# Performance work log

Measured on AMD Instinct MI355X. Metric: run time of the kernel, lower is better.

The kernel has to match this reference:

```python
import jax, jax.numpy as jnp
import numpy as np

B, M = 512, 2048            # batch of src-tgt pairs, sampled walk positions per pair
NUM_KEYS = 1_000_000        # unique (node, time) keys in nodetime2emb map
NUM_NODES = 100_000
LP = 4                      # num_layers + 1 (saw encoding width)
ENC = 32                    # enc_dim
FEAT = 64                   # node feature dim (MergeLayer dim2)
D3, D4 = 64, 1              # MergeLayer hidden / output dims


def setup_inputs() -> dict:
    key = jax.random.key(0)
    ks = jax.random.split(key, 12)
    s = 0.05
    return {
        "pos_table": jax.random.uniform(ks[0], (NUM_KEYS, LP), dtype=jnp.float32),
        "node_feat": jax.random.normal(ks[1], (NUM_NODES, FEAT), dtype=jnp.float32),
        "W1": jax.random.normal(ks[2], (LP, ENC), dtype=jnp.float32) * s,
        "b1": jnp.zeros((ENC,), dtype=jnp.float32),
        "W2": jax.random.normal(ks[3], (ENC, ENC), dtype=jnp.float32) * s,
        "b2": jnp.zeros((ENC,), dtype=jnp.float32),
        "Wm1": jax.random.normal(ks[4], (ENC + FEAT, D3), dtype=jnp.float32) * s,
        "bm1": jnp.zeros((D3,), dtype=jnp.float32),
        "Wm2": jax.random.normal(ks[5], (D3, D4), dtype=jnp.float32) * s,
        "bm2": jnp.zeros((D4,), dtype=jnp.float32),
        "key_idx": jax.random.randint(ks[6], (B, M), 0, NUM_KEYS, dtype=jnp.int32),
        "node_idx": jax.random.randint(ks[7], (B, M), 0, NUM_NODES, dtype=jnp.int32),
    }


def reference(pos_table, node_feat, W1, b1, W2, b2, Wm1, bm1, Wm2, bm2, key_idx, node_idx):
    # PositionEncoder.forward: gather saw encodings by (node, time) key,
    # then trainable_embedding = Linear(LP->ENC) -> ReLU -> Linear(ENC->ENC)
    enc = pos_table[key_idx]                       # [B, M, LP] irregular gather
    pe = jax.nn.relu(enc @ W1 + b1) @ W2 + b2      # [B, M, ENC]
    # gather raw node features for the same walk positions
    feat = node_feat[node_idx]                     # [B, M, FEAT] irregular gather
    # MergeLayer (non_linear=True): concat -> fc1 -> ReLU -> fc2
    x = jnp.concatenate([pe, feat], axis=-1)       # [B, M, ENC+FEAT]
    z = jax.nn.relu(x @ Wm1 + bm1) @ Wm2 + bm2     # [B, M, 1]
    return z
```

## Files before the change

kernel.cpp:

```cpp
#include <hip/hip_runtime.h>


typedef _Float16 half8 __attribute__((ext_vector_type(8)));
typedef float floatx4 __attribute__((ext_vector_type(4)));

#define HSTR 40
#define WSTR 104
#define GRID_MAIN 768

__global__ void feat_to_f16(const float* __restrict__ nf,
                            _Float16* __restrict__ o, int n8) {
    int t = blockIdx.x * 256 + threadIdx.x;
    if (t >= n8) return;
    const float4* p = (const float4*)nf + (size_t)t * 2;
    const float4 a = p[0], b = p[1];
    half8 h;
    h[0] = (_Float16)a.x; h[1] = (_Float16)a.y;
    h[2] = (_Float16)a.z; h[3] = (_Float16)a.w;
    h[4] = (_Float16)b.x; h[5] = (_Float16)b.y;
    h[6] = (_Float16)b.z; h[7] = (_Float16)b.w;
    *((half8*)o + t) = h;
}

__device__ __forceinline__ void load_feat(const _Float16* __restrict__ feat16,
                                          const float* __restrict__ node_feat,
                                          int use_f16, const int* ndr, int q,
                                          half8 fA[4][2]) {
    if (use_f16) {
        #pragma unroll
        for (int rt = 0; rt < 4; ++rt) {
            const _Float16* fb = feat16 + (size_t)ndr[rt] * 64 + q * 8;
            fA[rt][0] = *(const half8*)(fb);
            fA[rt][1] = *(const half8*)(fb + 32);
        }
    } else {
        #pragma unroll
        for (int rt = 0; rt < 4; ++rt) {
            const float* fb = node_feat + (size_t)ndr[rt] * 64 + q * 8;
            #pragma unroll
            for (int kt = 0; kt < 2; ++kt) {
                const float4 lo = *(const float4*)(fb + kt * 32);
                const float4 hi = *(const float4*)(fb + kt * 32 + 4);
                half8 h;
                h[0] = (_Float16)lo.x; h[1] = (_Float16)lo.y;
                h[2] = (_Float16)lo.z; h[3] = (_Float16)lo.w;
                h[4] = (_Float16)hi.x; h[5] = (_Float16)hi.y;
                h[6] = (_Float16)hi.z; h[7] = (_Float16)hi.w;
                fA[rt][kt] = h;
            }
        }
    }
}

__global__ __launch_bounds__(256, 3) void neurtw_r14(
    const float* __restrict__ pos_table,
    const float* __restrict__ node_feat,
    const float* __restrict__ W1,
    const float* __restrict__ b1,
    const float* __restrict__ W2,
    const float* __restrict__ b2,
    const float* __restrict__ Wm1,
    const float* __restrict__ bm1,
    const float* __restrict__ Wm2,
    const float* __restrict__ bm2,
    const int*   __restrict__ key_idx,
    const int*   __restrict__ node_idx,
    const _Float16* __restrict__ feat16,
    int use_f16,
    float*       __restrict__ out,
    int rows)
{
    __shared__ _Float16 hpe[256 * HSTR];
    __shared__ _Float16 wm1t[64 * WSTR];

    const int tid  = threadIdx.x;
    const int lane = tid & 63;
    const int r0   = (tid >> 6) * 64;
    const int ln   = lane & 15;
    const int q    = lane >> 4;

    #pragma unroll
    for (int i = 0; i < 3; ++i) {
        const int task = i * 256 + tid;
        const int n = task & 63, k8 = task >> 6;
        half8 w;
        #pragma unroll
        for (int kk = 0; kk < 8; ++kk)
            w[kk] = (_Float16)Wm1[(k8 * 8 + kk) * 64 + n];
        *(half8*)(&wm1t[n * WSTR + k8 * 8]) = w;
    }

    half8 b_w2[2];
    #pragma unroll
    for (int ct = 0; ct < 2; ++ct)
        #pragma unroll
        for (int j = 0; j < 8; ++j)
            b_w2[ct][j] = (_Float16)W2[(q * 8 + j) * 32 + ct * 16 + ln];
    float b2v[2];
    b2v[0] = b2[ln]; b2v[1] = b2[16 + ln];
    float bm1v[4], wm2v[4];
    #pragma unroll
    for (int ct = 0; ct < 4; ++ct) {
        bm1v[ct] = bm1[ct * 16 + ln];
        wm2v[ct] = Wm2[ct * 16 + ln];
    }
    const float bm2s = bm2[0];

    __syncthreads();

    int base = blockIdx.x * 256;
    int ndr[4];
    #pragma unroll
    for (int rt = 0; rt < 4; ++rt)
        ndr[rt] = node_idx[base + r0 + rt * 16 + ln];
    int kkc = key_idx[base + tid];
    float4 enc = *(const float4*)(pos_table + (size_t)kkc * 4);

    while (base < rows) {
        const int nbase = base + GRID_MAIN * 256;
        const bool more = nbase < rows;

        half8 fA[4][2];
        load_feat(feat16, node_feat, use_f16, ndr, q, fA);

        int ndr_n[4];
        int kk_n;
        if (more) {
            #pragma unroll
            for (int rt = 0; rt < 4; ++rt)
                ndr_n[rt] = node_idx[nbase + r0 + rt * 16 + ln];
            kk_n = key_idx[nbase + tid];
        } else {
            #pragma unroll
            for (int rt = 0; rt < 4; ++rt)
                ndr_n[rt] = 0;
            kk_n = 0;
        }

        #pragma unroll
        for (int g = 0; g < 4; ++g) {
            half8 hv;
            #pragma unroll
            for (int j8 = 0; j8 < 8; ++j8) {
                const int j = g * 8 + j8;
                float a = fmaf(enc.w, W1[96 + j],
                          fmaf(enc.z, W1[64 + j],
                          fmaf(enc.y, W1[32 + j],
                          fmaf(enc.x, W1[j], b1[j]))));
                hv[j8] = (_Float16)fmaxf(a, 0.0f);
            }
            *(half8*)(&hpe[tid * HSTR + g * 8]) = hv;
        }
        half8 a_h[4];
        #pragma unroll
        for (int rt = 0; rt < 4; ++rt)
            a_h[rt] = *(const half8*)(&hpe[(r0 + rt * 16 + ln) * HSTR + q * 8]);

        floatx4 pc[4][2];
        #pragma unroll
        for (int rt = 0; rt < 4; ++rt)
            #pragma unroll
            for (int ct = 0; ct < 2; ++ct) {
                floatx4 c = {0.f, 0.f, 0.f, 0.f};
                pc[rt][ct] = __builtin_amdgcn_mfma_f32_16x16x32_f16(
                    a_h[rt], b_w2[ct], c, 0, 0, 0);
            }

        #pragma unroll
        for (int rt = 0; rt < 4; ++rt)
            #pragma unroll
            for (int ct = 0; ct < 2; ++ct)
                #pragma unroll
                for (int r = 0; r < 4; ++r)
                    hpe[(r0 + rt * 16 + q * 4 + r) * HSTR + ct * 16 + ln] =
                        (_Float16)(pc[rt][ct][r] + b2v[ct]);

        float4 enc_n = enc;
        if (more)
            enc_n = *(const float4*)(pos_table + (size_t)kk_n * 4);

        floatx4 acc[4][4];
        #pragma unroll
        for (int ct = 0; ct < 4; ++ct) {
            const float bb = bm1v[ct];
            #pragma unroll
            for (int rt = 0; rt < 4; ++rt)
                acc[rt][ct] = (floatx4){bb, bb, bb, bb};
        }

        {
            half8 a_pe[4];
            #pragma unroll
            for (int rt = 0; rt < 4; ++rt)
                a_pe[rt] = *(const half8*)(&hpe[(r0 + rt * 16 + ln) * HSTR + q * 8]);
            half8 b0[4];
            #pragma unroll
            for (int ct = 0; ct < 4; ++ct)
                b0[ct] = *(const half8*)(&wm1t[(ct * 16 + ln) * WSTR + q * 8]);
            #pragma unroll
            for (int rt = 0; rt < 4; ++rt)
                #pragma unroll
                for (int ct = 0; ct < 4; ++ct)
                    acc[rt][ct] = __builtin_amdgcn_mfma_f32_16x16x32_f16(
                        a_pe[rt], b0[ct], acc[rt][ct], 0, 0, 0);
        }

        #pragma unroll
        for (int kt = 0; kt < 2; ++kt) {
            half8 bk[4];
            #pragma unroll
            for (int ct = 0; ct < 4; ++ct)
                bk[ct] = *(const half8*)(&wm1t[(ct * 16 + ln) * WSTR + 32 + kt * 32 + q * 8]);
            #pragma unroll
            for (int rt = 0; rt < 4; ++rt)
                #pragma unroll
                for (int ct = 0; ct < 4; ++ct)
                    acc[rt][ct] = __builtin_amdgcn_mfma_f32_16x16x32_f16(
                        fA[rt][kt], bk[ct], acc[rt][ct], 0, 0, 0);
        }

        #pragma unroll
        for (int rt = 0; rt < 4; ++rt) {
            #pragma unroll
            for (int r = 0; r < 4; ++r) {
                float p = 0.0f;
                #pragma unroll
                for (int ct = 0; ct < 4; ++ct)
                    p = fmaf(fmaxf(acc[rt][ct][r], 0.0f), wm2v[ct], p);
                p += __shfl_xor(p, 1);
                p += __shfl_xor(p, 2);
                p += __shfl_xor(p, 4);
                p += __shfl_xor(p, 8);
                if (ln == 0)
                    out[base + r0 + rt * 16 + q * 4 + r] = p + bm2s;
            }
        }

        base = nbase;
        #pragma unroll
        for (int rt = 0; rt < 4; ++rt)
            ndr[rt] = ndr_n[rt];
        kkc = kk_n;
        enc = enc_n;
    }
}

extern "C" void kernel_launch(void* const* d_in, const int* in_sizes, int n_in,
                              void* d_out, int out_size, void* d_ws, size_t ws_size,
                              hipStream_t stream) {
    const float* pos_table = (const float*)d_in[0];
    const float* node_feat = (const float*)d_in[1];
    const float* W1        = (const float*)d_in[2];
    const float* b1        = (const float*)d_in[3];
    const float* W2        = (const float*)d_in[4];
    const float* b2        = (const float*)d_in[5];
    const float* Wm1       = (const float*)d_in[6];
    const float* bm1       = (const float*)d_in[7];
    const float* Wm2       = (const float*)d_in[8];
    const float* bm2       = (const float*)d_in[9];
    const int*   key_idx   = (const int*)d_in[10];
    const int*   node_idx  = (const int*)d_in[11];
    float* out = (float*)d_out;

    const int rows  = in_sizes[10];
    const int nfeat = in_sizes[1];

    _Float16* feat16 = (_Float16*)d_ws;
    const size_t need = (size_t)nfeat * sizeof(_Float16);
    const int use_f16 = (ws_size >= need) ? 1 : 0;

    if (use_f16) {
        const int n8 = nfeat / 8;
        feat_to_f16<<<(n8 + 255) / 256, 256, 0, stream>>>(node_feat, feat16, n8);
    }

    neurtw_r14<<<GRID_MAIN, 256, 0, stream>>>(
        pos_table, node_feat, W1, b1, W2, b2, Wm1, bm1, Wm2, bm2,
        key_idx, node_idx, feat16, use_f16, out, rows);
}
```

Baseline: 156.8 us.

## Split MLP into two half-tiles to cut registers and raise occupancy

Splits the per-wave work of 4 row tiles into two passes of 2 row tiles, so the feature fragments and fc1 accumulators need only half the registers. The gather for the second half is issued in the middle of the first half's MFMAs. Launch bounds go from 3 to 4 waves per SIMD and the persistent grid from 768 to 1024 blocks, aiming to hide the random gather latency with more waves in flight. The cost is extra shared-memory B-fragment reloads and a more serialized instruction stream within each wave.

```diff
diff --git a/kernel.cpp b/kernel.cpp
--- a/kernel.cpp
+++ b/kernel.cpp
@@ -6,7 +6,7 @@
 
 #define HSTR 40
 #define WSTR 104
-#define GRID_MAIN 768
+#define GRID_MAIN 1024
 
 __global__ void feat_to_f16(const float* __restrict__ nf,
                             _Float16* __restrict__ o, int n8) {
@@ -22,21 +22,21 @@
     *((half8*)o + t) = h;
 }
 
-__device__ __forceinline__ void load_feat(const _Float16* __restrict__ feat16,
-                                          const float* __restrict__ node_feat,
-                                          int use_f16, const int* ndr, int q,
-                                          half8 fA[4][2]) {
+__device__ __forceinline__ void load_feat2(const _Float16* __restrict__ feat16,
+                                           const float* __restrict__ node_feat,
+                                           int use_f16, int nd0, int nd1, int q,
+                                           half8 fA[2][2]) {
     if (use_f16) {
-        #pragma unroll
-        for (int rt = 0; rt < 4; ++rt) {
-            const _Float16* fb = feat16 + (size_t)ndr[rt] * 64 + q * 8;
-            fA[rt][0] = *(const half8*)(fb);
-            fA[rt][1] = *(const half8*)(fb + 32);
-        }
+        const _Float16* fb0 = feat16 + (size_t)nd0 * 64 + q * 8;
+        const _Float16* fb1 = feat16 + (size_t)nd1 * 64 + q * 8;
+        fA[0][0] = *(const half8*)(fb0);
+        fA[0][1] = *(const half8*)(fb0 + 32);
+        fA[1][0] = *(const half8*)(fb1);
+        fA[1][1] = *(const half8*)(fb1 + 32);
     } else {
         #pragma unroll
-        for (int rt = 0; rt < 4; ++rt) {
-            const float* fb = node_feat + (size_t)ndr[rt] * 64 + q * 8;
+        for (int rr = 0; rr < 2; ++rr) {
+            const float* fb = node_feat + (size_t)(rr ? nd1 : nd0) * 64 + q * 8;
             #pragma unroll
             for (int kt = 0; kt < 2; ++kt) {
                 const float4 lo = *(const float4*)(fb + kt * 32);
@@ -46,13 +46,13 @@
                 h[2] = (_Float16)lo.z; h[3] = (_Float16)lo.w;
                 h[4] = (_Float16)hi.x; h[5] = (_Float16)hi.y;
                 h[6] = (_Float16)hi.z; h[7] = (_Float16)hi.w;
-                fA[rt][kt] = h;
+                fA[rr][kt] = h;
             }
         }
     }
 }
 
-__global__ __launch_bounds__(256, 3) void neurtw_r14(
+__global__ __launch_bounds__(256, 4) void neurtw_r15(
     const float* __restrict__ pos_table,
     const float* __restrict__ node_feat,
     const float* __restrict__ W1,
@@ -120,8 +120,8 @@
         const int nbase = base + GRID_MAIN * 256;
         const bool more = nbase < rows;
 
-        half8 fA[4][2];
-        load_feat(feat16, node_feat, use_f16, ndr, q, fA);
+        half8 fA[2][2];
+        load_feat2(feat16, node_feat, use_f16, ndr[0], ndr[1], q, fA);
 
         int ndr_n[4];
         int kk_n;
@@ -151,88 +151,132 @@
             }
             *(half8*)(&hpe[tid * HSTR + g * 8]) = hv;
         }
-        half8 a_h[4];
-        #pragma unroll
-        for (int rt = 0; rt < 4; ++rt)
-            a_h[rt] = *(const half8*)(&hpe[(r0 + rt * 16 + ln) * HSTR + q * 8]);
-
-        floatx4 pc[4][2];
-        #pragma unroll
-        for (int rt = 0; rt < 4; ++rt)
-            #pragma unroll
-            for (int ct = 0; ct < 2; ++ct) {
-                floatx4 c = {0.f, 0.f, 0.f, 0.f};
-                pc[rt][ct] = __builtin_amdgcn_mfma_f32_16x16x32_f16(
-                    a_h[rt], b_w2[ct], c, 0, 0, 0);
-            }
-
-        #pragma unroll
-        for (int rt = 0; rt < 4; ++rt)
-            #pragma unroll
-            for (int ct = 0; ct < 2; ++ct)
-                #pragma unroll
-                for (int r = 0; r < 4; ++r)
-                    hpe[(r0 + rt * 16 + q * 4 + r) * HSTR + ct * 16 + ln] =
-                        (_Float16)(pc[rt][ct][r] + b2v[ct]);
+
+        #pragma unroll
+        for (int rt = 0; rt < 4; ++rt) {
+            const half8 ah = *(const half8*)(&hpe[(r0 + rt * 16 + ln) * HSTR + q * 8]);
+            floatx4 z0 = {0.f, 0.f, 0.f, 0.f};
+            floatx4 z1 = {0.f, 0.f, 0.f, 0.f};
+            const floatx4 p0 = __builtin_amdgcn_mfma_f32_16x16x32_f16(ah, b_w2[0], z0, 0, 0, 0);
+            const floatx4 p1 = __builtin_amdgcn_mfma_f32_16x16x32_f16(ah, b_w2[1], z1, 0, 0, 0);
+            #pragma unroll
+            for (int r = 0; r < 4; ++r) {
+                hpe[(r0 + rt * 16 + q * 4 + r) * HSTR + ln]      = (_Float16)(p0[r] + b2v[0]);
+                hpe[(r0 + rt * 16 + q * 4 + r) * HSTR + 16 + ln] = (_Float16)(p1[r] + b2v[1]);
+            }
+        }
 
         float4 enc_n = enc;
         if (more)
             enc_n = *(const float4*)(pos_table + (size_t)kk_n * 4);
 
-        floatx4 acc[4][4];
+        floatx4 acc[2][4];
+
         #pragma unroll
         for (int ct = 0; ct < 4; ++ct) {
             const float bb = bm1v[ct];
-            #pragma unroll
-            for (int rt = 0; rt < 4; ++rt)
-                acc[rt][ct] = (floatx4){bb, bb, bb, bb};
-        }
+            acc[0][ct] = (floatx4){bb, bb, bb, bb};
+            acc[1][ct] = (floatx4){bb, bb, bb, bb};
+        }
+
+        #pragma unroll
+        for (int kt = 0; kt < 2; ++kt) {
+            half8 bk[4];
+            #pragma unroll
+            for (int ct = 0; ct < 4; ++ct)
+                bk[ct] = *(const half8*)(&wm1t[(ct * 16 + ln) * WSTR + 32 + kt * 32 + q * 8]);
+            #pragma unroll
+            for (int rr = 0; rr < 2; ++rr)
+                #pragma unroll
+                for (int ct = 0; ct < 4; ++ct)
+                    acc[rr][ct] = __builtin_amdgcn_mfma_f32_16x16x32_f16(
+                        fA[rr][kt], bk[ct], acc[rr][ct], 0, 0, 0);
+        }
+
+        load_feat2(feat16, node_feat, use_f16, ndr[2], ndr[3], q, fA);
 
         {
-            half8 a_pe[4];
-            #pragma unroll
-            for (int rt = 0; rt < 4; ++rt)
-                a_pe[rt] = *(const half8*)(&hpe[(r0 + rt * 16 + ln) * HSTR + q * 8]);
             half8 b0[4];
             #pragma unroll
             for (int ct = 0; ct < 4; ++ct)
                 b0[ct] = *(const half8*)(&wm1t[(ct * 16 + ln) * WSTR + q * 8]);
             #pragma unroll
-            for (int rt = 0; rt < 4; ++rt)
-                #pragma unroll
-                for (int ct = 0; ct < 4; ++ct)
-                    acc[rt][ct] = __builtin_amdgcn_mfma_f32_16x16x32_f16(
-                        a_pe[rt], b0[ct], acc[rt][ct], 0, 0, 0);
-        }
-
-        #pragma unroll
-        for (int kt = 0; kt < 2; ++kt) {
-            half8 bk[4];
-            #pragma unroll
-            for (int ct = 0; ct < 4; ++ct)
-                bk[ct] = *(const half8*)(&wm1t[(ct * 16 + ln) * WSTR + 32 + kt * 32 + q * 8]);
-            #pragma unroll
-            for (int rt = 0; rt < 4; ++rt)
-                #pragma unroll
-                for (int ct = 0; ct < 4; ++ct)
-                    acc[rt][ct] = __builtin_amdgcn_mfma_f32_16x16x32_f16(
-                        fA[rt][kt], bk[ct], acc[rt][ct], 0, 0, 0);
-        }
-
-        #pragma unroll
-        for (int rt = 0; rt < 4; ++rt) {
+            for (int rr = 0; rr < 2; ++rr) {
+                const half8 ap = *(const half8*)(&hpe[(r0 + rr * 16 + ln) * HSTR + q * 8]);
+                #pragma unroll
+                for (int ct = 0; ct < 4; ++ct)
+                    acc[rr][ct] = __builtin_amdgcn_mfma_f32_16x16x32_f16(
+                        ap, b0[ct], acc[rr][ct], 0, 0, 0);
+            }
+        }
+
+        #pragma unroll
+        for (int rr = 0; rr < 2; ++rr) {
             #pragma unroll
             for (int r = 0; r < 4; ++r) {
                 float p = 0.0f;
                 #pragma unroll
                 for (int ct = 0; ct < 4; ++ct)
-                    p = fmaf(fmaxf(acc[rt][ct][r], 0.0f), wm2v[ct], p);
+                    p = fmaf(fmaxf(acc[rr][ct][r], 0.0f), wm2v[ct], p);
                 p += __shfl_xor(p, 1);
                 p += __shfl_xor(p, 2);
                 p += __shfl_xor(p, 4);
                 p += __shfl_xor(p, 8);
                 if (ln == 0)
-                    out[base + r0 + rt * 16 + q * 4 + r] = p + bm2s;
+                    out[base + r0 + rr * 16 + q * 4 + r] = p + bm2s;
+            }
+        }
+
+        #pragma unroll
+        for (int ct = 0; ct < 4; ++ct) {
+            const float bb = bm1v[ct];
+            acc[0][ct] = (floatx4){bb, bb, bb, bb};
+            acc[1][ct] = (floatx4){bb, bb, bb, bb};
+        }
+
+        {
+            half8 b0[4];
+            #pragma unroll
+            for (int ct = 0; ct < 4; ++ct)
+                b0[ct] = *(const half8*)(&wm1t[(ct * 16 + ln) * WSTR + q * 8]);
+            #pragma unroll
+            for (int rr = 0; rr < 2; ++rr) {
+                const half8 ap = *(const half8*)(&hpe[(r0 + (2 + rr) * 16 + ln) * HSTR + q * 8]);
+                #pragma unroll
+                for (int ct = 0; ct < 4; ++ct)
+                    acc[rr][ct] = __builtin_amdgcn_mfma_f32_16x16x32_f16(
+                        ap, b0[ct], acc[rr][ct], 0, 0, 0);
+            }
+        }
+
+        #pragma unroll
+        for (int kt = 0; kt < 2; ++kt) {
+            half8 bk[4];
+            #pragma unroll
+            for (int ct = 0; ct < 4; ++ct)
+                bk[ct] = *(const half8*)(&wm1t[(ct * 16 + ln) * WSTR + 32 + kt * 32 + q * 8]);
+            #pragma unroll
+            for (int rr = 0; rr < 2; ++rr)
+                #pragma unroll
+                for (int ct = 0; ct < 4; ++ct)
+                    acc[rr][ct] = __builtin_amdgcn_mfma_f32_16x16x32_f16(
+                        fA[rr][kt], bk[ct], acc[rr][ct], 0, 0, 0);
+        }
+
+        #pragma unroll
+        for (int rr = 0; rr < 2; ++rr) {
+            #pragma unroll
+            for (int r = 0; r < 4; ++r) {
+                float p = 0.0f;
+                #pragma unroll
+                for (int ct = 0; ct < 4; ++ct)
+                    p = fmaf(fmaxf(acc[rr][ct][r], 0.0f), wm2v[ct], p);
+                p += __shfl_xor(p, 1);
+                p += __shfl_xor(p, 2);
+                p += __shfl_xor(p, 4);
+                p += __shfl_xor(p, 8);
+                if (ln == 0)
+                    out[base + r0 + (2 + rr) * 16 + q * 4 + r] = p + bm2s;
             }
         }
 
@@ -274,7 +318,7 @@
         feat_to_f16<<<(n8 + 255) / 256, 256, 0, stream>>>(node_feat, feat16, n8);
     }
 
-    neurtw_r14<<<GRID_MAIN, 256, 0, stream>>>(
+    neurtw_r15<<<GRID_MAIN, 256, 0, stream>>>(
         pos_table, node_feat, W1, b1, W2, b2, Wm1, bm1, Wm2, bm2,
         key_idx, node_idx, feat16, use_f16, out, rows);
 }
```

Result: slower. 177.7 us (+13.3%).
